# Performance work log

Measured on AMD Instinct MI355X. Metric: run time of the kernel, lower is better.

Reference implementation:

```python
import jax, jax.numpy as jnp
import numpy as np

T, B, D, H, O = 512, 256, 1024, 1024, 5


def setup_inputs() -> dict:
    key = jax.random.key(0)
    ks = jax.random.split(key, 7)
    s = 1.0 / np.sqrt(H).astype(np.float32)
    u = lambda k, shape: jax.random.uniform(k, shape, jnp.float32, -s, s)
    return {
        "input": jax.random.normal(ks[0], (T, B, D), jnp.float32),
        "hidden": jnp.zeros((B, H), jnp.float32),
        "state": jnp.zeros((B, H), jnp.float32),
        "W_in": u(ks[1], (H, D)),   # input_scale (Linear(hidden,hidden); D==H)
        "b_in": u(ks[2], (H,)),
        "W_h": u(ks[3], (H, H)),    # hidden_scale
        "b_h": u(ks[4], (H,)),
        "W_o": u(ks[5], (O, H)),    # h2o
        "b_o": u(ks[6], (O,)),
    }


def reference(input, hidden, state, W_in, b_in, W_h, b_h, W_o, b_o):
    # Dropout(0.5) is identity in eval mode.
    # Per timestep: h = sigmoid(hidden_scale(h) + input_scale(x_t))
    def step(h, x_t):
        e = x_t @ W_in.T + b_in              # [B, H]
        h = jax.nn.sigmoid(h @ W_h.T + b_h + e)
        return h, None

    hidden, _ = jax.lax.scan(step, hidden, input)  # scan over T
    out = jax.nn.log_softmax(hidden @ W_o.T + b_o, axis=-1)  # [B, O]
    return (out, hidden, state)
```

## Files before the change

### kernel.cpp

```cpp
#include <hip/hip_runtime.h>

#define T_STEPS 512
#define BATCH   256
#define DIM     1024
#define NOUT    5
#define BH      (BATCH*DIM)
#define TB      (T_STEPS*BATCH)

typedef short s16x8 __attribute__((ext_vector_type(8)));
typedef float f32x4 __attribute__((ext_vector_type(4)));
typedef unsigned short u16;
typedef unsigned int   u32;

__device__ __forceinline__ u16 f2bf(float f) {
    union { float f; u32 u; } v; v.f = f;
    u32 r = v.u + 0x7FFFu + ((v.u >> 16) & 1u);
    return (u16)(r >> 16);
}
__device__ __forceinline__ float bf2f(u16 u) {
    union { u32 u; float f; } v; v.u = ((u32)u) << 16;
    return v.f;
}
__device__ __forceinline__ s16x8 cvt8(float4 a, float4 b) {
    s16x8 v;
    v[0]=(short)f2bf(a.x); v[1]=(short)f2bf(a.y); v[2]=(short)f2bf(a.z); v[3]=(short)f2bf(a.w);
    v[4]=(short)f2bf(b.x); v[5]=(short)f2bf(b.y); v[6]=(short)f2bf(b.z); v[7]=(short)f2bf(b.w);
    return v;
}

__device__ __forceinline__ void ldg_cv16_issue(const u16* p, s16x8* dst) {
    asm volatile("global_load_dwordx4 %0, %1, off sc0 sc1"
                 : "=v"(*dst) : "v"(p) : "memory");
}
__device__ __forceinline__ void stg_cv8(u16* p, ushort4 v) {
    asm volatile("global_store_dwordx2 %0, %1, off sc0 sc1"
                 :: "v"(p), "v"(v) : "memory");
}
__device__ __forceinline__ void stg_cv4(u32* p, u32 v) {
    asm volatile("global_store_dword %0, %1, off sc0 sc1"
                 :: "v"(p), "v"(v) : "memory");
}
__device__ __forceinline__ void wait_vm0() {
    asm volatile("s_waitcnt vmcnt(0)" ::: "memory");
}

__global__ __launch_bounds__(256) void cvt_kernel(const float* __restrict__ src,
                                                  u16* __restrict__ dst, int n4) {
    int i = blockIdx.x * 256 + threadIdx.x;
    if (i < n4) {
        float4 x = ((const float4*)src)[i];
        ushort4 o;
        o.x = f2bf(x.x); o.y = f2bf(x.y); o.z = f2bf(x.z); o.w = f2bf(x.w);
        ((ushort4*)dst)[i] = o;
    }
}

__global__ __launch_bounds__(256) void cvt_x(const float* __restrict__ src,
                                             u16* __restrict__ dst, int n8) {
    int i = blockIdx.x * 256 + threadIdx.x;
    if (i < n8) {
        float4 a = ((const float4*)src)[2*i];
        float4 b = ((const float4*)src)[2*i + 1];
        *(s16x8*)&dst[(size_t)i*8] = cvt8(a, b);
    }
}

__global__ __launch_bounds__(256, 2) void gemm_e_bf(
    const u16*   __restrict__ Xb,
    const u16*   __restrict__ Wb,
    const float* __restrict__ b_in,
    u16*         __restrict__ E)
{
    __shared__ u16 sA[128 * 64];
    __shared__ u16 sB[128 * 64];

    const int K = 1024;
    int tid  = threadIdx.x;
    int lane = tid & 63, wv = tid >> 6;
    int lm   = lane & 15, quad = lane >> 4;

    int bid = blockIdx.x;
    int xcd = bid & 7;
    int s   = bid >> 3;
    int bn  = s & 7;
    int bm  = (s >> 3) * 8 + xcd;

    int wm = wv >> 1, wn = wv & 1;

    float bias[4];
#pragma unroll
    for (int nt = 0; nt < 4; ++nt)
        bias[nt] = b_in[bn*128 + wn*64 + nt*16 + lm];

    f32x4 acc[4][4];
#pragma unroll
    for (int a = 0; a < 4; ++a)
#pragma unroll
        for (int b = 0; b < 4; ++b)
            acc[a][b] = (f32x4){0.f, 0.f, 0.f, 0.f};

    int colX  = (lane & 7) ^ (lane >> 3);
    int rowX0 = lane >> 3;

    for (int kk = 0; kk < K; kk += 64) {
#pragma unroll
        for (int i = 0; i < 4; ++i) {
            int q   = i*4 + wv;
            int row = q*8 + rowX0;
            const u16* gpB = Wb + (size_t)(bn*128 + row)*K + kk + colX*8;
            __builtin_amdgcn_global_load_lds(
                (const __attribute__((address_space(1))) void*)gpB,
                (__attribute__((address_space(3))) void*)(sB + q*512),
                16, 0, 0);
            const u16* gpA = Xb + (size_t)(bm*128 + row)*K + kk + colX*8;
            __builtin_amdgcn_global_load_lds(
                (const __attribute__((address_space(1))) void*)gpA,
                (__attribute__((address_space(3))) void*)(sA + q*512),
                16, 0, 0);
        }
        __syncthreads();
#pragma unroll
        for (int kc = 0; kc < 2; ++kc) {
            s16x8 af[4], bfr[4];
            int c8 = kc*4 + quad;
#pragma unroll
            for (int mt = 0; mt < 4; ++mt) {
                int row = wm*64 + mt*16 + lm;
                af[mt] = *(const s16x8*)&sA[row*64 + ((c8 ^ (row & 7)) * 8)];
            }
#pragma unroll
            for (int nt = 0; nt < 4; ++nt) {
                int row = wn*64 + nt*16 + lm;
                bfr[nt] = *(const s16x8*)&sB[row*64 + ((c8 ^ (row & 7)) * 8)];
            }
#pragma unroll
            for (int mt = 0; mt < 4; ++mt)
#pragma unroll
                for (int nt = 0; nt < 4; ++nt)
                    acc[mt][nt] = __builtin_amdgcn_mfma_f32_16x16x32_bf16(
                        af[mt], bfr[nt], acc[mt][nt], 0, 0, 0);
        }
        __syncthreads();
    }
#pragma unroll
    for (int mt = 0; mt < 4; ++mt)
#pragma unroll
        for (int nt = 0; nt < 4; ++nt)
#pragma unroll
            for (int i = 0; i < 4; ++i) {
                int row = bm*128 + wm*64 + mt*16 + quad*4 + i;
                int col = bn*128 + wn*64 + nt*16 + lm;
                E[(size_t)row*1024 + col] = f2bf(acc[mt][nt][i] + bias[nt]);
            }
}

#define PADA 88

__global__ __launch_bounds__(256, 2) void gemm_e(
    const float* __restrict__ X,
    const u16*   __restrict__ Wb,
    const float* __restrict__ b_in,
    u16*         __restrict__ E)
{
    __shared__ u16 sA[128 * PADA];
    __shared__ u16 sB[128 * 64];

    const int K = 1024;
    int tid  = threadIdx.x;
    int lane = tid & 63, wv = tid >> 6;
    int lm   = lane & 15, quad = lane >> 4;

    int bid = blockIdx.x;
    int xcd = bid & 7;
    int s   = bid >> 3;
    int bn  = s & 7;
    int bm  = (s >> 3) * 8 + xcd;

    int wm = wv >> 1, wn = wv & 1;

    float bias[4];
#pragma unroll
    for (int nt = 0; nt < 4; ++nt)
        bias[nt] = b_in[bn*128 + wn*64 + nt*16 + lm];

    f32x4 acc[4][4];
#pragma unroll
    for (int a = 0; a < 4; ++a)
#pragma unroll
        for (int b = 0; b < 4; ++b)
            acc[a][b] = (f32x4){0.f, 0.f, 0.f, 0.f};

    int colB  = (lane & 7) ^ (lane >> 3);
    int rowB0 = lane >> 3;

    for (int kk = 0; kk < K; kk += 64) {
#pragma unroll
        for (int i = 0; i < 4; ++i) {
            int q   = i*4 + wv;
            int row = q*8 + rowB0;
            const u16* gp = Wb + (size_t)(bn*128 + row)*K + kk + colB*8;
            __builtin_amdgcn_global_load_lds(
                (const __attribute__((address_space(1))) void*)gp,
                (__attribute__((address_space(3))) void*)(sB + q*512),
                16, 0, 0);
        }
#pragma unroll
        for (int p = 0; p < 4; ++p) {
            int row = (tid >> 3) + 32*p;
            int k8  = (tid & 7) * 8;
            const float* gp = X + (size_t)(bm*128 + row)*K + kk + k8;
            float4 x0 = ((const float4*)gp)[0];
            float4 x1 = ((const float4*)gp)[1];
            *(s16x8*)&sA[row*PADA + k8] = cvt8(x0, x1);
        }
        __syncthreads();
#pragma unroll
        for (int kc = 0; kc < 2; ++kc) {
            s16x8 af[4], bfr[4];
#pragma unroll
            for (int mt = 0; mt < 4; ++mt) {
                int row = wm*64 + mt*16 + lm;
                af[mt] = *(const s16x8*)&sA[row*PADA + kc*32 + quad*8];
            }
            int c8 = kc*4 + quad;
#pragma unroll
            for (int nt = 0; nt < 4; ++nt) {
                int row = wn*64 + nt*16 + lm;
                bfr[nt] = *(const s16x8*)&sB[row*64 + ((c8 ^ (row & 7)) * 8)];
            }
#pragma unroll
            for (int mt = 0; mt < 4; ++mt)
#pragma unroll
                for (int nt = 0; nt < 4; ++nt)
                    acc[mt][nt] = __builtin_amdgcn_mfma_f32_16x16x32_bf16(
                        af[mt], bfr[nt], acc[mt][nt], 0, 0, 0);
        }
        __syncthreads();
    }
#pragma unroll
    for (int mt = 0; mt < 4; ++mt)
#pragma unroll
        for (int nt = 0; nt < 4; ++nt)
#pragma unroll
            for (int i = 0; i < 4; ++i) {
                int row = bm*128 + wm*64 + mt*16 + quad*4 + i;
                int col = bn*128 + wn*64 + nt*16 + lm;
                E[(size_t)row*1024 + col] = f2bf(acc[mt][nt][i] + bias[nt]);
            }
}

__global__ __launch_bounds__(256, 1) void rnn_phase2(
    const float* __restrict__ h0,
    const float* __restrict__ Wh,
    const float* __restrict__ bh,
    const u16*   __restrict__ E,
    u16*         __restrict__ hbuf,
    u32*         __restrict__ flags,
    float*       __restrict__ hidden_out)
{
    __shared__ float red[2][4][16][68];
    int tid  = threadIdx.x;
    int lane = tid & 63, wv = tid >> 6;
    int lm   = lane & 15, quad = lane >> 4;
    int r    = blockIdx.x >> 4, c = blockIdx.x & 15;

    s16x8 wf[4][8];
#pragma unroll
    for (int ct = 0; ct < 4; ++ct)
#pragma unroll
        for (int kc = 0; kc < 8; ++kc) {
            int n = c*64 + ct*16 + lm;
            int k = wv*256 + kc*32 + quad*8;
            const float* p = Wh + (size_t)n*1024 + k;
            float4 x0 = ((const float4*)p)[0];
            float4 x1 = ((const float4*)p)[1];
            wf[ct][kc] = cvt8(x0, x1);
        }

    int m  = tid >> 4;
    int n4 = (tid & 15) * 4;
    float4 bh4 = *(const float4*)&bh[c*64 + n4];
    int rowA = r*16 + lm;
    const u32* fpoll = flags + (size_t)(r*16 + wv*4 + (lane & 3))*16 + ((lane >> 2) & 3)*4;
    u32* fown = flags + (size_t)(r*16 + c)*16 + wv*4;

    for (int t = 0; t < T_STEPS; ++t) {
        if (t > 0) {
            u32 target = (u32)t;
            for (;;) {
                u32 v;
                asm volatile("global_load_dword %0, %1, off sc0 sc1"
                             : "=v"(v) : "v"(fpoll) : "memory");
                asm volatile("s_waitcnt vmcnt(0)" ::: "memory");
                if (__all(v >= target)) break;
                __builtin_amdgcn_s_sleep(1);
            }
        }

        ushort4 e4 = *(const ushort4*)&E[(size_t)t*BH + (size_t)(r*16 + m)*1024 + c*64 + n4];

        s16x8 af[8];
        if (t == 0) {
#pragma unroll
            for (int kc = 0; kc < 8; ++kc) {
                const float* p = h0 + (size_t)rowA*1024 + wv*256 + kc*32 + quad*8;
                float4 x0 = ((const float4*)p)[0];
                float4 x1 = ((const float4*)p)[1];
                af[kc] = cvt8(x0, x1);
            }
        } else {
            const u16* hb = hbuf + (size_t)(t & 1)*BH;
#pragma unroll
            for (int kc = 0; kc < 8; ++kc)
                ldg_cv16_issue(&hb[(size_t)rowA*1024 + wv*256 + kc*32 + quad*8], &af[kc]);
            asm volatile("s_waitcnt vmcnt(0)"
                         : "+v"(af[0]), "+v"(af[1]), "+v"(af[2]), "+v"(af[3]),
                           "+v"(af[4]), "+v"(af[5]), "+v"(af[6]), "+v"(af[7])
                         :: "memory");
        }

        f32x4 acc[4];
#pragma unroll
        for (int ct = 0; ct < 4; ++ct) acc[ct] = (f32x4){0.f, 0.f, 0.f, 0.f};
#pragma unroll
        for (int kc = 0; kc < 8; ++kc)
#pragma unroll
            for (int ct = 0; ct < 4; ++ct)
                acc[ct] = __builtin_amdgcn_mfma_f32_16x16x32_bf16(af[kc], wf[ct][kc], acc[ct], 0, 0, 0);

#pragma unroll
        for (int ct = 0; ct < 4; ++ct)
#pragma unroll
            for (int i = 0; i < 4; ++i)
                red[t & 1][wv][quad*4 + i][ct*16 + lm] = acc[ct][i];
        __syncthreads();

        float4 p0 = *(const float4*)&red[t & 1][0][m][n4];
        float4 p1 = *(const float4*)&red[t & 1][1][m][n4];
        float4 p2 = *(const float4*)&red[t & 1][2][m][n4];
        float4 p3 = *(const float4*)&red[t & 1][3][m][n4];
        float4 s;
        s.x = p0.x + p1.x + p2.x + p3.x + bh4.x + bf2f(e4.x);
        s.y = p0.y + p1.y + p2.y + p3.y + bh4.y + bf2f(e4.y);
        s.z = p0.z + p1.z + p2.z + p3.z + bh4.z + bf2f(e4.z);
        s.w = p0.w + p1.w + p2.w + p3.w + bh4.w + bf2f(e4.w);
        float4 h;
        h.x = 1.f / (1.f + __expf(-s.x));
        h.y = 1.f / (1.f + __expf(-s.y));
        h.z = 1.f / (1.f + __expf(-s.z));
        h.w = 1.f / (1.f + __expf(-s.w));

        if (t < T_STEPS - 1) {
            ushort4 hb4;
            hb4.x = f2bf(h.x); hb4.y = f2bf(h.y); hb4.z = f2bf(h.z); hb4.w = f2bf(h.w);
            stg_cv8(&hbuf[(size_t)((t + 1) & 1)*BH + (size_t)(r*16 + m)*1024 + c*64 + n4], hb4);
        } else {
            *(float4*)&hidden_out[(size_t)(r*16 + m)*1024 + c*64 + n4] = h;
        }

        wait_vm0();
        if (lane == 0 && t < T_STEPS - 1)
            stg_cv4(fown, (u32)(t + 1));
    }
}

__global__ __launch_bounds__(64) void head_kernel(const float* __restrict__ h,
                                                  const float* __restrict__ Wo,
                                                  const float* __restrict__ bo,
                                                  float* __restrict__ out)
{
    int b = blockIdx.x, l = threadIdx.x;
    float a0 = 0.f, a1 = 0.f, a2 = 0.f, a3 = 0.f, a4 = 0.f;
    for (int k = l; k < DIM; k += 64) {
        float hv = h[b*DIM + k];
        a0 += hv * Wo[0*DIM + k];
        a1 += hv * Wo[1*DIM + k];
        a2 += hv * Wo[2*DIM + k];
        a3 += hv * Wo[3*DIM + k];
        a4 += hv * Wo[4*DIM + k];
    }
#pragma unroll
    for (int off = 32; off >= 1; off >>= 1) {
        a0 += __shfl_down(a0, off);
        a1 += __shfl_down(a1, off);
        a2 += __shfl_down(a2, off);
        a3 += __shfl_down(a3, off);
        a4 += __shfl_down(a4, off);
    }
    if (l == 0) {
        float v[5] = {a0 + bo[0], a1 + bo[1], a2 + bo[2], a3 + bo[3], a4 + bo[4]};
        float mx = v[0];
#pragma unroll
        for (int o = 1; o < 5; ++o) mx = fmaxf(mx, v[o]);
        float sum = 0.f;
#pragma unroll
        for (int o = 0; o < 5; ++o) sum += __expf(v[o] - mx);
        float lse = mx + __logf(sum);
#pragma unroll
        for (int o = 0; o < 5; ++o) out[b*NOUT + o] = v[o] - lse;
    }
}

extern "C" void kernel_launch(void* const* d_in, const int* in_sizes, int n_in,
                              void* d_out, int out_size, void* d_ws, size_t ws_size,
                              hipStream_t stream)
{
    const float* X   = (const float*)d_in[0];
    const float* h0  = (const float*)d_in[1];
    const float* st  = (const float*)d_in[2];
    const float* Win = (const float*)d_in[3];
    const float* bin = (const float*)d_in[4];
    const float* Wh  = (const float*)d_in[5];
    const float* bhp = (const float*)d_in[6];
    const float* Wo  = (const float*)d_in[7];
    const float* bo  = (const float*)d_in[8];

    char*  ws      = (char*)d_ws;
    size_t off_hb  = 32768;
    size_t off_wb  = off_hb + (size_t)2*BH*2;
    size_t off_e   = off_wb + (size_t)DIM*DIM*2;
    size_t off_xb  = off_e + (size_t)TB*DIM*2;
    size_t need_bf = off_xb + (size_t)TB*DIM*2;

    u32* flags = (u32*)ws;
    u16* hbuf  = (u16*)(ws + off_hb);
    u16* Wbf   = (u16*)(ws + off_wb);
    u16* E     = (u16*)(ws + off_e);
    u16* Xbf   = (u16*)(ws + off_xb);

    float* out_lp = (float*)d_out;
    float* out_h  = out_lp + BATCH*NOUT;
    float* out_st = out_h + BH;

    hipMemsetAsync(flags, 0, 32768, stream);
    cvt_kernel<<<(DIM*DIM/4 + 255)/256, 256, 0, stream>>>(Win, Wbf, DIM*DIM/4);

    if (ws_size >= need_bf) {
        cvt_x<<<(TB*DIM/8)/256, 256, 0, stream>>>(X, Xbf, TB*DIM/8);
        gemm_e_bf<<<(TB/128)*8, 256, 0, stream>>>(Xbf, Wbf, bin, E);
    } else {
        gemm_e<<<(TB/128)*8, 256, 0, stream>>>(X, Wbf, bin, E);
    }

    rnn_phase2<<<256, 256, 0, stream>>>(h0, Wh, bhp, E, hbuf, flags, out_h);
    head_kernel<<<BATCH, 64, 0, stream>>>(out_h, Wo, bo, out_lp);
    hipMemcpyAsync(out_st, st, (size_t)BH*sizeof(float), hipMemcpyDeviceToDevice, stream);
}
```

Before: 2.857 ms.

## Embed step parity in bf16 sign bits to replace flag-based cross-block sync

```diff
diff --git a/kernel.cpp b/kernel.cpp
--- a/kernel.cpp
+++ b/kernel.cpp
@@ -9,8 +9,10 @@
 
 typedef short s16x8 __attribute__((ext_vector_type(8)));
 typedef float f32x4 __attribute__((ext_vector_type(4)));
+typedef unsigned int u32;
 typedef unsigned short u16;
-typedef unsigned int   u32;
+typedef u32 u32x4 __attribute__((ext_vector_type(4)));
+typedef u32 u32x2 __attribute__((ext_vector_type(2)));
 
 __device__ __forceinline__ u16 f2bf(float f) {
     union { float f; u32 u; } v; v.f = f;
@@ -28,20 +30,13 @@
     return v;
 }
 
-__device__ __forceinline__ void ldg_cv16_issue(const u16* p, s16x8* dst) {
+__device__ __forceinline__ void ldg_cv16_issue(const u16* p, u32x4* dst) {
     asm volatile("global_load_dwordx4 %0, %1, off sc0 sc1"
                  : "=v"(*dst) : "v"(p) : "memory");
 }
-__device__ __forceinline__ void stg_cv8(u16* p, ushort4 v) {
+__device__ __forceinline__ void stg_cv8_u32(u16* p, u32x2 v) {
     asm volatile("global_store_dwordx2 %0, %1, off sc0 sc1"
                  :: "v"(p), "v"(v) : "memory");
-}
-__device__ __forceinline__ void stg_cv4(u32* p, u32 v) {
-    asm volatile("global_store_dword %0, %1, off sc0 sc1"
-                 :: "v"(p), "v"(v) : "memory");
-}
-__device__ __forceinline__ void wait_vm0() {
-    asm volatile("s_waitcnt vmcnt(0)" ::: "memory");
 }
 
 __global__ __launch_bounds__(256) void cvt_kernel(const float* __restrict__ src,
@@ -71,8 +66,9 @@
     const float* __restrict__ b_in,
     u16*         __restrict__ E)
 {
-    __shared__ u16 sA[128 * 64];
-    __shared__ u16 sB[128 * 64];
+    __shared__ u16 smem[2 * 128 * 64];
+    u16* sA = smem;
+    u16* sB = smem + 128 * 64;
 
     const int K = 1024;
     int tid  = threadIdx.x;
@@ -142,16 +138,26 @@
         }
         __syncthreads();
     }
+
 #pragma unroll
     for (int mt = 0; mt < 4; ++mt)
 #pragma unroll
         for (int nt = 0; nt < 4; ++nt)
 #pragma unroll
             for (int i = 0; i < 4; ++i) {
-                int row = bm*128 + wm*64 + mt*16 + quad*4 + i;
-                int col = bn*128 + wn*64 + nt*16 + lm;
-                E[(size_t)row*1024 + col] = f2bf(acc[mt][nt][i] + bias[nt]);
-            }
+                int row = wm*64 + mt*16 + quad*4 + i;
+                int col = wn*64 + nt*16 + lm;
+                smem[row*128 + col] = f2bf(acc[mt][nt][i] + bias[nt]);
+            }
+    __syncthreads();
+#pragma unroll
+    for (int sIt = 0; sIt < 8; ++sIt) {
+        int flat = sIt*4096 + tid*16;
+        int row  = flat >> 8;
+        int colb = flat & 255;
+        s16x8 v = *(const s16x8*)((const char*)smem + flat);
+        *(s16x8*)&E[(size_t)(bm*128 + row)*1024 + bn*128 + colb/2] = v;
+    }
 }
 
 #define PADA 88
@@ -255,7 +261,6 @@
     const float* __restrict__ bh,
     const u16*   __restrict__ E,
     u16*         __restrict__ hbuf,
-    u32*         __restrict__ flags,
     float*       __restrict__ hidden_out)
 {
     __shared__ float red[2][4][16][68];
@@ -281,52 +286,55 @@
     int n4 = (tid & 15) * 4;
     float4 bh4 = *(const float4*)&bh[c*64 + n4];
     int rowA = r*16 + lm;
-    const u32* fpoll = flags + (size_t)(r*16 + wv*4 + (lane & 3))*16 + ((lane >> 2) & 3)*4;
-    u32* fown = flags + (size_t)(r*16 + c)*16 + wv*4;
+    size_t aoff = (size_t)rowA*1024 + wv*256 + quad*8;
+    size_t soff = (size_t)(r*16 + m)*1024 + c*64 + n4;
 
     for (int t = 0; t < T_STEPS; ++t) {
-        if (t > 0) {
-            u32 target = (u32)t;
-            for (;;) {
-                u32 v;
-                asm volatile("global_load_dword %0, %1, off sc0 sc1"
-                             : "=v"(v) : "v"(fpoll) : "memory");
-                asm volatile("s_waitcnt vmcnt(0)" ::: "memory");
-                if (__all(v >= target)) break;
-                __builtin_amdgcn_s_sleep(1);
-            }
-        }
-
-        ushort4 e4 = *(const ushort4*)&E[(size_t)t*BH + (size_t)(r*16 + m)*1024 + c*64 + n4];
-
-        s16x8 af[8];
+        ushort4 e4 = *(const ushort4*)&E[(size_t)t*BH + soff];
+
+        u32x4 afu[8];
         if (t == 0) {
 #pragma unroll
             for (int kc = 0; kc < 8; ++kc) {
-                const float* p = h0 + (size_t)rowA*1024 + wv*256 + kc*32 + quad*8;
+                const float* p = h0 + aoff + kc*32;
                 float4 x0 = ((const float4*)p)[0];
                 float4 x1 = ((const float4*)p)[1];
-                af[kc] = cvt8(x0, x1);
+                afu[kc] = __builtin_bit_cast(u32x4, cvt8(x0, x1));
             }
         } else {
             const u16* hb = hbuf + (size_t)(t & 1)*BH;
+            u32 s2 = (u32)t & 3u;
+            u32 expect = ((s2 & 1u) ? 0x8000u : 0u) | ((s2 & 2u) ? 0x80000000u : 0u);
+            for (;;) {
+#pragma unroll
+                for (int kc = 0; kc < 8; ++kc)
+                    ldg_cv16_issue(hb + aoff + kc*32, &afu[kc]);
+                asm volatile("s_waitcnt vmcnt(0)"
+                             : "+v"(afu[0]), "+v"(afu[1]), "+v"(afu[2]), "+v"(afu[3]),
+                               "+v"(afu[4]), "+v"(afu[5]), "+v"(afu[6]), "+v"(afu[7])
+                             :: "memory");
+                u32x4 bad4 = (u32x4){0u, 0u, 0u, 0u};
+#pragma unroll
+                for (int kc = 0; kc < 8; ++kc)
+                    bad4 |= (afu[kc] ^ expect) & 0x80008000u;
+                u32 bad = bad4[0] | bad4[1] | bad4[2] | bad4[3];
+                if (__all(bad == 0u)) break;
+            }
 #pragma unroll
             for (int kc = 0; kc < 8; ++kc)
-                ldg_cv16_issue(&hb[(size_t)rowA*1024 + wv*256 + kc*32 + quad*8], &af[kc]);
-            asm volatile("s_waitcnt vmcnt(0)"
-                         : "+v"(af[0]), "+v"(af[1]), "+v"(af[2]), "+v"(af[3]),
-                           "+v"(af[4]), "+v"(af[5]), "+v"(af[6]), "+v"(af[7])
-                         :: "memory");
+                afu[kc] &= 0x7FFF7FFFu;
         }
 
         f32x4 acc[4];
 #pragma unroll
         for (int ct = 0; ct < 4; ++ct) acc[ct] = (f32x4){0.f, 0.f, 0.f, 0.f};
 #pragma unroll
-        for (int kc = 0; kc < 8; ++kc)
+        for (int kc = 0; kc < 8; ++kc) {
+            s16x8 a = __builtin_bit_cast(s16x8, afu[kc]);
 #pragma unroll
             for (int ct = 0; ct < 4; ++ct)
-                acc[ct] = __builtin_amdgcn_mfma_f32_16x16x32_bf16(af[kc], wf[ct][kc], acc[ct], 0, 0, 0);
+                acc[ct] = __builtin_amdgcn_mfma_f32_16x16x32_bf16(a, wf[ct][kc], acc[ct], 0, 0, 0);
+        }
 
 #pragma unroll
         for (int ct = 0; ct < 4; ++ct)
@@ -339,28 +347,27 @@
         float4 p1 = *(const float4*)&red[t & 1][1][m][n4];
         float4 p2 = *(const float4*)&red[t & 1][2][m][n4];
         float4 p3 = *(const float4*)&red[t & 1][3][m][n4];
-        float4 s;
-        s.x = p0.x + p1.x + p2.x + p3.x + bh4.x + bf2f(e4.x);
-        s.y = p0.y + p1.y + p2.y + p3.y + bh4.y + bf2f(e4.y);
-        s.z = p0.z + p1.z + p2.z + p3.z + bh4.z + bf2f(e4.z);
-        s.w = p0.w + p1.w + p2.w + p3.w + bh4.w + bf2f(e4.w);
+        float4 sv;
+        sv.x = p0.x + p1.x + p2.x + p3.x + bh4.x + bf2f(e4.x);
+        sv.y = p0.y + p1.y + p2.y + p3.y + bh4.y + bf2f(e4.y);
+        sv.z = p0.z + p1.z + p2.z + p3.z + bh4.z + bf2f(e4.z);
+        sv.w = p0.w + p1.w + p2.w + p3.w + bh4.w + bf2f(e4.w);
         float4 h;
-        h.x = 1.f / (1.f + __expf(-s.x));
-        h.y = 1.f / (1.f + __expf(-s.y));
-        h.z = 1.f / (1.f + __expf(-s.z));
-        h.w = 1.f / (1.f + __expf(-s.w));
+        h.x = 1.f / (1.f + __expf(-sv.x));
+        h.y = 1.f / (1.f + __expf(-sv.y));
+        h.z = 1.f / (1.f + __expf(-sv.z));
+        h.w = 1.f / (1.f + __expf(-sv.w));
 
         if (t < T_STEPS - 1) {
-            ushort4 hb4;
-            hb4.x = f2bf(h.x); hb4.y = f2bf(h.y); hb4.z = f2bf(h.z); hb4.w = f2bf(h.w);
-            stg_cv8(&hbuf[(size_t)((t + 1) & 1)*BH + (size_t)(r*16 + m)*1024 + c*64 + n4], hb4);
+            u32 s3   = (u32)(t + 1) & 3u;
+            u32 mask = ((s3 & 1u) ? 0x8000u : 0u) | ((s3 & 2u) ? 0x80000000u : 0u);
+            u32x2 st;
+            st[0] = ((u32)f2bf(h.x) | ((u32)f2bf(h.y) << 16)) | mask;
+            st[1] = ((u32)f2bf(h.z) | ((u32)f2bf(h.w) << 16)) | mask;
+            stg_cv8_u32(&hbuf[(size_t)((t + 1) & 1)*BH + soff], st);
         } else {
-            *(float4*)&hidden_out[(size_t)(r*16 + m)*1024 + c*64 + n4] = h;
-        }
-
-        wait_vm0();
-        if (lane == 0 && t < T_STEPS - 1)
-            stg_cv4(fown, (u32)(t + 1));
+            *(float4*)&hidden_out[soff] = h;
+        }
     }
 }
 
@@ -422,7 +429,6 @@
     size_t off_xb  = off_e + (size_t)TB*DIM*2;
     size_t need_bf = off_xb + (size_t)TB*DIM*2;
 
-    u32* flags = (u32*)ws;
     u16* hbuf  = (u16*)(ws + off_hb);
     u16* Wbf   = (u16*)(ws + off_wb);
     u16* E     = (u16*)(ws + off_e);
@@ -432,7 +438,7 @@
     float* out_h  = out_lp + BATCH*NOUT;
     float* out_st = out_h + BH;
 
-    hipMemsetAsync(flags, 0, 32768, stream);
+    hipMemsetAsync(hbuf, 0, (size_t)2*BH*2, stream);
     cvt_kernel<<<(DIM*DIM/4 + 255)/256, 256, 0, stream>>>(Win, Wbf, DIM*DIM/4);
 
     if (ws_size >= need_bf) {
@@ -442,7 +448,7 @@
         gemm_e<<<(TB/128)*8, 256, 0, stream>>>(X, Wbf, bin, E);
     }
 
-    rnn_phase2<<<256, 256, 0, stream>>>(h0, Wh, bhp, E, hbuf, flags, out_h);
+    rnn_phase2<<<256, 256, 0, stream>>>(h0, Wh, bhp, E, hbuf, out_h);
     head_kernel<<<BATCH, 64, 0, stream>>>(out_h, Wo, bo, out_lp);
     hipMemcpyAsync(out_st, st, (size_t)BH*sizeof(float), hipMemcpyDeviceToDevice, stream);
 }
```

Result: faster. 2.653 ms (-7.2%).
